# Kernel tuning notes

Measured on AMD Instinct MI355X. Metric: run time of the kernel, lower is better.

## Reference

```python
import jax, jax.numpy as jnp
import numpy as np

UP = 2          # up_factor
FLT = 4         # flt_dim
CH = 64
# pad from UpFirDn2D.__init__ (up branch): pad = FLT - UP = 2
PAD0 = (FLT - UP + 1) // 2 + UP - 1   # 2
PAD1 = (FLT - UP) // 2                # 1


def make_filter(channels=CH, size=FLT, scale=UP):
    # binomial 1D kernel for size=4: [1,3,3,1]
    k1 = jnp.array([1.0, 3.0, 3.0, 1.0], dtype=jnp.float32)
    k = k1[None, :] * k1[:, None]
    k = k / k.sum()
    k = k * (scale ** 2)
    # depthwise kernel, OIHW with I=1, repeated per channel
    return jnp.broadcast_to(k[None, None, :, :], (channels, 1, size, size))


def setup_inputs() -> dict:
    key = jax.random.key(0)
    x = jax.random.normal(key, (16, CH, 128, 128), dtype=jnp.float32)
    filt = make_filter()
    return {"x": x, "filt": filt}


def reference(x, filt):
    # Fused upfirdn2d: zero-interleave upsample (PixelShuffle with zero pads
    # == lhs_dilation=UP; the pixel-shuffle's trailing zero row/col plus
    # F.pad's (PAD0 left/top, PAD1 right/bottom) equals symmetric padding
    # (PAD0, PAD1 + UP - 1) on the dilated grid), then depthwise 4x4 FIR,
    # no downsample (dn_factor=1).
    b, c, h, w = x.shape
    pad = (PAD0, PAD1 + (UP - 1))  # (2, 2)
    y = jax.lax.conv_general_dilated(
        x, filt,
        window_strides=(1, 1),
        padding=(pad, pad),
        lhs_dilation=(UP, UP),
        feature_group_count=c,
        dimension_numbers=("NCHW", "OIHW", "NCHW"),
    )
    return y  # (b, c, h*UP, w*UP)
```

## Files before the change

### kernel.cpp

```cpp
#include <hip/hip_runtime.h>


constexpr int H = 128, W = 128, WO = 256;

__global__ __launch_bounds__(256) void upfirdn2d_up2(
    const float* __restrict__ x, const float* __restrict__ f,
    float* __restrict__ y) {
  const int j  = threadIdx.x;
  const int i  = blockIdx.x * 4 + threadIdx.y;
  const int bc = blockIdx.y;
  const int c  = bc & 63;

  float k[16];
  const float* kp = f + c * 16;
#pragma unroll
  for (int t = 0; t < 16; ++t) k[t] = kp[t];

  const float* xin = x + (size_t)bc * (H * W);
  float*       yo  = y + (size_t)bc * (WO * WO);

  float r[3][4];
#pragma unroll
  for (int t = 0; t < 3; ++t) {
    const int row = i - 1 + t;
    const bool rok = ((unsigned)row < (unsigned)H);
    const float* rp = xin + row * W;
    float2 mid = rok ? *(const float2*)(rp + 2 * j) : make_float2(0.f, 0.f);
    r[t][0] = (rok && j > 0)  ? rp[2 * j - 1] : 0.f;
    r[t][1] = mid.x;
    r[t][2] = mid.y;
    r[t][3] = (rok && j < 63) ? rp[2 * j + 2] : 0.f;
  }

  float4 o0, o1;
  o0.x = k[0]*r[0][0] + k[2]*r[0][1] + k[8] *r[1][0] + k[10]*r[1][1];
  o0.y = k[1]*r[0][1] + k[3]*r[0][2] + k[9] *r[1][1] + k[11]*r[1][2];
  o0.z = k[0]*r[0][1] + k[2]*r[0][2] + k[8] *r[1][1] + k[10]*r[1][2];
  o0.w = k[1]*r[0][2] + k[3]*r[0][3] + k[9] *r[1][2] + k[11]*r[1][3];

  o1.x = k[4]*r[1][0] + k[6]*r[1][1] + k[12]*r[2][0] + k[14]*r[2][1];
  o1.y = k[5]*r[1][1] + k[7]*r[1][2] + k[13]*r[2][1] + k[15]*r[2][2];
  o1.z = k[4]*r[1][1] + k[6]*r[1][2] + k[12]*r[2][1] + k[14]*r[2][2];
  o1.w = k[5]*r[1][2] + k[7]*r[1][3] + k[13]*r[2][2] + k[15]*r[2][3];

  float4* p0 = (float4*)(yo + (size_t)(2 * i)     * WO + 4 * j);
  float4* p1 = (float4*)(yo + (size_t)(2 * i + 1) * WO + 4 * j);
  *p0 = o0;
  *p1 = o1;
}

extern "C" void kernel_launch(void* const* d_in, const int* in_sizes, int n_in,
                              void* d_out, int out_size, void* d_ws, size_t ws_size,
                              hipStream_t stream) {
  const float* x = (const float*)d_in[0];
  const float* f = (const float*)d_in[1];
  float*       y = (float*)d_out;

  dim3 block(64, 4);
  dim3 grid(32, 1024);
  hipLaunchKernelGGL(upfirdn2d_up2, grid, block, 0, stream, x, f, y);
}
```

Baseline: 329.8 us.

## Process two input rows per thread, use wave shuffles and nontemporal stores

Each thread now produces four output rows from two input rows, loading 4 input rows instead of 3 per 2 rows, which halves the grid and reduces redundant row loads. Neighbour columns come from wavefront shuffles instead of extra scalar global loads, and outputs are written with nontemporal stores to avoid polluting cache with the 256 MB write stream. The cost is fewer threads in flight and more registers per thread.

```diff
diff --git a/kernel.cpp b/kernel.cpp
--- a/kernel.cpp
+++ b/kernel.cpp
@@ -3,11 +3,13 @@
 
 constexpr int H = 128, W = 128, WO = 256;
 
+typedef float vfloat4 __attribute__((ext_vector_type(4)));
+
 __global__ __launch_bounds__(256) void upfirdn2d_up2(
     const float* __restrict__ x, const float* __restrict__ f,
     float* __restrict__ y) {
   const int j  = threadIdx.x;
-  const int i  = blockIdx.x * 4 + threadIdx.y;
+  const int q  = blockIdx.x * 4 + threadIdx.y;
   const int bc = blockIdx.y;
   const int c  = bc & 63;
 
@@ -19,34 +21,41 @@
   const float* xin = x + (size_t)bc * (H * W);
   float*       yo  = y + (size_t)bc * (WO * WO);
 
-  float r[3][4];
+  float a[4][4];
 #pragma unroll
-  for (int t = 0; t < 3; ++t) {
-    const int row = i - 1 + t;
+  for (int t = 0; t < 4; ++t) {
+    const int row = 2 * q - 1 + t;
     const bool rok = ((unsigned)row < (unsigned)H);
-    const float* rp = xin + row * W;
-    float2 mid = rok ? *(const float2*)(rp + 2 * j) : make_float2(0.f, 0.f);
-    r[t][0] = (rok && j > 0)  ? rp[2 * j - 1] : 0.f;
-    r[t][1] = mid.x;
-    r[t][2] = mid.y;
-    r[t][3] = (rok && j < 63) ? rp[2 * j + 2] : 0.f;
+    float2 mid = rok ? *(const float2*)(xin + row * W + 2 * j)
+                     : make_float2(0.f, 0.f);
+    const float left  = __shfl_up(mid.y, 1);
+    const float right = __shfl_down(mid.x, 1);
+    a[t][0] = (j == 0)  ? 0.f : left;
+    a[t][1] = mid.x;
+    a[t][2] = mid.y;
+    a[t][3] = (j == 63) ? 0.f : right;
   }
 
-  float4 o0, o1;
-  o0.x = k[0]*r[0][0] + k[2]*r[0][1] + k[8] *r[1][0] + k[10]*r[1][1];
-  o0.y = k[1]*r[0][1] + k[3]*r[0][2] + k[9] *r[1][1] + k[11]*r[1][2];
-  o0.z = k[0]*r[0][1] + k[2]*r[0][2] + k[8] *r[1][1] + k[10]*r[1][2];
-  o0.w = k[1]*r[0][2] + k[3]*r[0][3] + k[9] *r[1][2] + k[11]*r[1][3];
+  auto frow = [&](const float* kr, const float (&u)[4],
+                  const float* ks, const float (&v)[4]) -> vfloat4 {
+    vfloat4 o;
+    o.x = kr[0]*u[0] + kr[2]*u[1] + ks[0]*v[0] + ks[2]*v[1];
+    o.y = kr[1]*u[1] + kr[3]*u[2] + ks[1]*v[1] + ks[3]*v[2];
+    o.z = kr[0]*u[1] + kr[2]*u[2] + ks[0]*v[1] + ks[2]*v[2];
+    o.w = kr[1]*u[2] + kr[3]*u[3] + ks[1]*v[2] + ks[3]*v[3];
+    return o;
+  };
 
-  o1.x = k[4]*r[1][0] + k[6]*r[1][1] + k[12]*r[2][0] + k[14]*r[2][1];
-  o1.y = k[5]*r[1][1] + k[7]*r[1][2] + k[13]*r[2][1] + k[15]*r[2][2];
-  o1.z = k[4]*r[1][1] + k[6]*r[1][2] + k[12]*r[2][1] + k[14]*r[2][2];
-  o1.w = k[5]*r[1][2] + k[7]*r[1][3] + k[13]*r[2][2] + k[15]*r[2][3];
+  const vfloat4 o0 = frow(k + 0, a[0], k + 8,  a[1]);
+  const vfloat4 o1 = frow(k + 4, a[1], k + 12, a[2]);
+  const vfloat4 o2 = frow(k + 0, a[1], k + 8,  a[2]);
+  const vfloat4 o3 = frow(k + 4, a[2], k + 12, a[3]);
 
-  float4* p0 = (float4*)(yo + (size_t)(2 * i)     * WO + 4 * j);
-  float4* p1 = (float4*)(yo + (size_t)(2 * i + 1) * WO + 4 * j);
-  *p0 = o0;
-  *p1 = o1;
+  float* base = yo + (size_t)(4 * q) * WO + 4 * j;
+  __builtin_nontemporal_store(o0, (vfloat4*)(base));
+  __builtin_nontemporal_store(o1, (vfloat4*)(base + WO));
+  __builtin_nontemporal_store(o2, (vfloat4*)(base + 2 * WO));
+  __builtin_nontemporal_store(o3, (vfloat4*)(base + 3 * WO));
 }
 
 extern "C" void kernel_launch(void* const* d_in, const int* in_sizes, int n_in,
@@ -57,6 +66,6 @@
   float*       y = (float*)d_out;
 
   dim3 block(64, 4);
-  dim3 grid(32, 1024);
+  dim3 grid(16, 1024);
   hipLaunchKernelGGL(upfirdn2d_up2, grid, block, 0, stream, x, f, y);
 }
```

Measured after the change: 306.0 us. 1.08x faster.
